# Optimization experiments

Hardware: AMD Instinct MI355X
Metric: run time of the kernel (lower is better)

## Reference

```python
import jax, jax.numpy as jnp
import numpy as np

B, S, D, H = 2, 2048, 512, 8
DK = D // H  # 64


def setup_inputs() -> dict:
    key = jax.random.key(0)
    ks = jax.random.split(key, 16)
    def t(k):
        return jax.random.normal(k, (B, S, D), dtype=jnp.float32)
    inp = {
        'query_real': t(ks[0]), 'key_real': t(ks[1]), 'value_real': t(ks[2]),
        'query_phase': t(ks[3]), 'key_phase': t(ks[4]), 'value_phase': t(ks[5]),
        'mask': jax.random.randint(ks[6], (B, 1, S), 0, 2, dtype=jnp.int32),
    }
    # Four distinct linear layers (clones deepcopies); real and phase paths share them.
    for i, nm in enumerate(['q', 'k', 'v', 'o']):
        inp['W' + nm] = jax.random.normal(ks[7 + 2 * i], (D, D), dtype=jnp.float32) * 0.02
        inp['b' + nm] = jax.random.normal(ks[8 + 2 * i], (D,), dtype=jnp.float32) * 0.02
    return inp


def _lin(x, W, b):
    # nn.Linear: x @ W.T + b
    return jnp.einsum('bsd,ed->bse', x, W) + b


def _heads(x):
    # [B,S,D] -> [B,H,S,DK]
    return jnp.swapaxes(x.reshape(B, S, H, DK), 1, 2)


def reference(query_real, key_real, value_real, query_phase, key_phase, value_phase,
              mask, Wq, bq, Wk, bk, Wv, bv, Wo, bo):
    qr = _heads(_lin(query_real, Wq, bq)); qp = _heads(_lin(query_phase, Wq, bq))
    kr = _heads(_lin(key_real, Wk, bk));   kp = _heads(_lin(key_phase, Wk, bk))
    vr = _heads(_lin(value_real, Wv, bv)); vp = _heads(_lin(value_phase, Wv, bv))

    # complex QK^T: 4 matmuls -> real/imag parts, magnitude score
    sr = jnp.einsum('bhqd,bhkd->bhqk', qr, kr) - jnp.einsum('bhqd,bhkd->bhqk', qp, kp)
    sp = jnp.einsum('bhqd,bhkd->bhqk', qr, kp) + jnp.einsum('bhqd,bhkd->bhqk', qp, kr)
    scores = jnp.sqrt(sr * sr + sp * sp) / jnp.sqrt(jnp.float32(DK))
    # mask [B,1,S] -> unsqueeze head dim -> [B,1,1,S]
    scores = jnp.where(mask[:, None] == 0, jnp.float32(-1e9), scores)
    p = jax.nn.softmax(scores, axis=-1)

    xr = jnp.einsum('bhqk,bhkd->bhqd', p, vr)
    xp = jnp.einsum('bhqk,bhkd->bhqd', p, vp)
    xr = jnp.swapaxes(xr, 1, 2).reshape(B, S, D)
    xp = jnp.swapaxes(xp, 1, 2).reshape(B, S, D)
    return _lin(xr, Wo, bo), _lin(xp, Wo, bo)
```

## Files before the change

### kernel.cpp

```cpp
#include <hip/hip_runtime.h>

typedef __bf16 bf16;
typedef __bf16 bf16x8 __attribute__((ext_vector_type(8)));
typedef float  f32x4  __attribute__((ext_vector_type(4)));

static constexpr int CB = 2;
static constexpr int CS = 2048;
static constexpr int CD = 512;
static constexpr int CH = 8;
static constexpr int CDK = 64;
static constexpr int NROWS = CB * CH * CS;
static constexpr size_t NT = (size_t)CB * CS * CD;
static constexpr size_t WN = (size_t)CD * CD;

__device__ __forceinline__ f32x4 mfma16(bf16x8 a, bf16x8 b, f32x4 c) {
    return __builtin_amdgcn_mfma_f32_16x16x32_bf16(a, b, c, 0, 0, 0);
}

__device__ __forceinline__ bf16x8 cvt8(const float* __restrict__ p) {
    float4 x0 = *reinterpret_cast<const float4*>(p);
    float4 x1 = *reinterpret_cast<const float4*>(p + 4);
    bf16x8 r;
    r[0] = (bf16)x0.x; r[1] = (bf16)x0.y; r[2] = (bf16)x0.z; r[3] = (bf16)x0.w;
    r[4] = (bf16)x1.x; r[5] = (bf16)x1.y; r[6] = (bf16)x1.z; r[7] = (bf16)x1.w;
    return r;
}

__device__ __forceinline__ void gload16(const void* g, void* l) {
    __builtin_amdgcn_global_load_lds(
        (const __attribute__((address_space(1))) void*)g,
        (__attribute__((address_space(3))) void*)l, 16, 0, 0);
}

struct CvtP {
    const float* src[10];
    bf16* dst[10];
    int n8[10];
};
__global__ __launch_bounds__(256) void cvt_kernel(CvtP C) {
    const int t = blockIdx.y;
    const int i = blockIdx.x * 256 + threadIdx.x;
    if (i < C.n8[t])
        *reinterpret_cast<bf16x8*>(C.dst[t] + (size_t)i * 8) =
            cvt8(C.src[t] + (size_t)i * 8);
}

struct PB {
    const bf16* A[6];
    const bf16* W[6];
    const float* bias[6];
    bf16* dst[6];
    int mode[6];
};
__global__ __launch_bounds__(256) void projb_kernel(PB P) {
    __shared__ uint4 tile[2][2][512];

    const int z = blockIdx.z;
    const bf16* __restrict__ A = P.A[z];
    const bf16* __restrict__ W = P.W[z];
    const float* __restrict__ bias = P.bias[z];
    bf16* __restrict__ dst = P.dst[z];
    const int mode = P.mode[z];

    const int m0 = blockIdx.x * 128, n0 = blockIdx.y * 128;
    const int tid = threadIdx.x;
    const int lane = tid & 63, w = tid >> 6;
    const int wr = w >> 1, wc = w & 1;
    const int l16 = lane & 15, lhi = lane >> 4;

    const int tensor = w >> 1, half = w & 1;
    const int rlo = lane >> 2, ch = lane & 3;
    const bf16* gbase = tensor ? W : A;
    const int t0 = tensor ? n0 : m0;
    const char* gp = (const char*)gbase
                   + (size_t)(t0 + half*64 + rlo) * (CD * 2)
                   + (size_t)((ch ^ (rlo & 3)) * 16);

    auto stage = [&](int buf, int kk) {
        const char* p = gp + (size_t)kk * 64;
        uint4* ld = &tile[buf][tensor][half * 256];
        #pragma unroll
        for (int i = 0; i < 4; ++i)
            gload16(p + (size_t)i * 16 * (CD * 2), ld + i * 64);
    };

    f32x4 acc[4][4] = {};

    stage(0, 0);
    asm volatile("s_waitcnt vmcnt(0)" ::: "memory");
    __syncthreads();

    for (int kk = 0; kk < 16; ++kk) {
        if (kk + 1 < 16) stage((kk + 1) & 1, kk + 1);

        const uint4* aT = &tile[kk & 1][0][0];
        const uint4* bT = &tile[kk & 1][1][0];
        bf16x8 af[4], bg[4];
        #pragma unroll
        for (int ms = 0; ms < 4; ++ms) {
            const int ra = wr*64 + ms*16 + l16;
            af[ms] = __builtin_bit_cast(bf16x8, aT[ra*4 + (lhi ^ (ra & 3))]);
        }
        #pragma unroll
        for (int ns = 0; ns < 4; ++ns) {
            const int rb = wc*64 + ns*16 + l16;
            bg[ns] = __builtin_bit_cast(bf16x8, bT[rb*4 + (lhi ^ (rb & 3))]);
        }
        #pragma unroll
        for (int ms = 0; ms < 4; ++ms)
            #pragma unroll
            for (int ns = 0; ns < 4; ++ns)
                acc[ms][ns] = mfma16(af[ms], bg[ns], acc[ms][ns]);

        if (kk + 1 < 16) __syncthreads();
    }

    #pragma unroll
    for (int ms = 0; ms < 4; ++ms)
    #pragma unroll
    for (int ns = 0; ns < 4; ++ns) {
        const int col = n0 + wc*64 + ns*16 + l16;
        const float bv = bias[col];
        const int hh = col >> 6, dk = col & 63;
        #pragma unroll
        for (int i = 0; i < 4; ++i) {
            const int m = m0 + wr*64 + ms*16 + lhi*4 + i;
            const float v = acc[ms][ns][i] + bv;
            const int b = m >> 11, s = m & 2047;
            if (mode == 0)
                dst[(((size_t)(b*CH + hh)) * CS + s) * CDK + dk] = (bf16)v;
            else
                dst[(((size_t)(b*CH + hh)) * CDK + dk) * CS + s] = (bf16)v;
        }
    }
}

__global__ __launch_bounds__(256) void oprojb_kernel(
    const bf16* __restrict__ Xr, const bf16* __restrict__ Xp,
    const bf16* __restrict__ Wo, const float* __restrict__ bo,
    float* __restrict__ out)
{
    __shared__ uint4 tile[2][2][512];

    const bf16* __restrict__ A = blockIdx.z ? Xp : Xr;
    float* __restrict__ dst = out + (size_t)blockIdx.z * NT;

    const int m0 = blockIdx.x * 64, n0 = blockIdx.y * 64;
    const int tid = threadIdx.x;
    const int lane = tid & 63, w = tid >> 6;
    const int wm = w >> 1, wn = w & 1;
    const int l16 = lane & 15, lhi = lane >> 4;

    const int tensor = w >> 1, half = w & 1;
    const int rlo = lane >> 3, slotL = lane & 7;
    const bf16* gbase = tensor ? Wo : A;
    const int t0 = tensor ? n0 : m0;
    const char* gp = (const char*)gbase
                   + (size_t)(t0 + half*32 + rlo) * (CD * 2)
                   + (size_t)((slotL ^ rlo) * 16);

    auto stage = [&](int buf, int kk) {
        const char* p = gp + (size_t)kk * 128;
        uint4* ld = &tile[buf][tensor][half * 256];
        #pragma unroll
        for (int i = 0; i < 4; ++i)
            gload16(p + (size_t)i * 8 * (CD * 2), ld + i * 64);
    };

    f32x4 acc[2][2] = {};

    stage(0, 0);
    asm volatile("s_waitcnt vmcnt(0)" ::: "memory");
    __syncthreads();

    for (int kk = 0; kk < 8; ++kk) {
        if (kk + 1 < 8) stage((kk + 1) & 1, kk + 1);

        const uint4* aT = &tile[kk & 1][0][0];
        const uint4* bT = &tile[kk & 1][1][0];
        #pragma unroll
        for (int ks = 0; ks < 2; ++ks) {
            const int c = ks*4 + lhi;
            const int ra0 = wm*32 + l16, ra1 = ra0 + 16;
            const int rb0 = wn*32 + l16, rb1 = rb0 + 16;
            bf16x8 af0 = __builtin_bit_cast(bf16x8, aT[ra0*8 + (c ^ (ra0 & 7))]);
            bf16x8 af1 = __builtin_bit_cast(bf16x8, aT[ra1*8 + (c ^ (ra1 & 7))]);
            bf16x8 bg0 = __builtin_bit_cast(bf16x8, bT[rb0*8 + (c ^ (rb0 & 7))]);
            bf16x8 bg1 = __builtin_bit_cast(bf16x8, bT[rb1*8 + (c ^ (rb1 & 7))]);
            acc[0][0] = mfma16(af0, bg0, acc[0][0]);
            acc[0][1] = mfma16(af0, bg1, acc[0][1]);
            acc[1][0] = mfma16(af1, bg0, acc[1][0]);
            acc[1][1] = mfma16(af1, bg1, acc[1][1]);
        }
        if (kk + 1 < 8) __syncthreads();
    }

    #pragma unroll
    for (int ms = 0; ms < 2; ++ms)
    #pragma unroll
    for (int ns = 0; ns < 2; ++ns) {
        const int col = n0 + wn*32 + ns*16 + l16;
        const float bv = bo[col];
        #pragma unroll
        for (int i = 0; i < 4; ++i) {
            const int m = m0 + wm*32 + ms*16 + lhi*4 + i;
            dst[(size_t)m * 512 + col] = acc[ms][ns][i] + bv;
        }
    }
}

__global__ __launch_bounds__(512, 4) void attn_kernel(
    const bf16* __restrict__ Qr, const bf16* __restrict__ Qp,
    const bf16* __restrict__ Kr, const bf16* __restrict__ Kp,
    const bf16* __restrict__ Vtr, const bf16* __restrict__ Vtp,
    const int* __restrict__ mask, int lognsp,
    float* __restrict__ POR, float* __restrict__ POP, float* __restrict__ PLs)
{
    __shared__ uint4 stg[2][4][512];

    const int F = blockIdx.x;
    const int qt = (F >> 3) & 15;
    const int g  = (F & 7) | ((F >> 7) << 3);
    const int bh = g >> lognsp, z = g & ((1 << lognsp) - 1);
    const int Lkv = CS >> lognsp, kvbase = z * Lkv;
    const int nt = Lkv >> 6;
    const int b = bh >> 3;
    const size_t base = (size_t)bh * CS * CDK;

    const int tid = threadIdx.x, lane = tid & 63, w = tid >> 6;
    const int l16 = lane & 15, lhi = lane >> 4;
    const int q0 = qt * 128 + w * 16;

    const int tensor = w >> 1, half = w & 1;
    const int rlo = lane >> 3, slotL = lane & 7;
    const int chunkL = slotL ^ rlo;
    const char* gsrc = (tensor == 0) ? (const char*)Kr : (tensor == 1) ? (const char*)Kp
                     : (tensor == 2) ? (const char*)Vtr : (const char*)Vtp;
    size_t laneoff, iStride, tStride;
    if (tensor < 2) {
        laneoff = base*2 + (size_t)(kvbase + half*32 + rlo) * 128 + chunkL*16;
        iStride = 8 * 128;  tStride = 8192;
    } else {
        laneoff = base*2 + (size_t)(half*32 + rlo) * (CS*2) + (size_t)kvbase*2 + chunkL*16;
        iStride = 8 * CS * 2;  tStride = 128;
    }
    const char* gp = gsrc + laneoff;

    auto stage = [&](int bi, int t) {
        const char* p = gp + (size_t)t * tStride;
        uint4* ldst = &stg[bi][tensor][half * 256];
        #pragma unroll
        for (int i = 0; i < 4; ++i)
            gload16(p + i*iStride, ldst + i*64);
    };

    stage(0, 0);

    bf16x8 qrf[2], qpf[2], qnf[2];
    #pragma unroll
    for (int ks = 0; ks < 2; ++ks) {
        const size_t qoff = base + (size_t)(q0 + l16) * CDK + ks*32 + lhi*8;
        qrf[ks] = *reinterpret_cast<const bf16x8*>(&Qr[qoff]);
        qpf[ks] = *reinterpret_cast<const bf16x8*>(&Qp[qoff]);
        uint4 t = __builtin_bit_cast(uint4, qpf[ks]);
        t.x ^= 0x80008000u; t.y ^= 0x80008000u; t.z ^= 0x80008000u; t.w ^= 0x80008000u;
        qnf[ks] = __builtin_bit_cast(bf16x8, t);
    }

    unsigned long long keepA[8] = {};
    for (int t = 0; t < nt; ++t) {
        const unsigned long long m64 =
            __ballot(mask[b*CS + kvbase + t*64 + lane] != 0);
        const unsigned long long s = m64 >> (lhi * 4);
        const unsigned int k16 = (unsigned int)(s & 0xFull)
                               | ((unsigned int)((s >> 16) & 0xFull) << 4)
                               | ((unsigned int)((s >> 32) & 0xFull) << 8)
                               | ((unsigned int)((s >> 48) & 0xFull) << 12);
        keepA[t >> 2] |= (unsigned long long)k16 << ((t & 3) * 16);
    }

    f32x4 oR[4] = {}, oP[4] = {};
    float lpart = 0.f;

    asm volatile("s_waitcnt vmcnt(0)" ::: "memory");
    __syncthreads();

    for (int t = 0; t < nt; ++t) {
        if (t + 1 < nt) stage((t + 1) & 1, t + 1);

        const int bi = t & 1;
        const unsigned int k16 = (unsigned int)(keepA[t >> 2] >> ((t & 3) * 16)) & 0xFFFFu;
        const uint4* kTr = &stg[bi][0][0];
        const uint4* kTp = &stg[bi][1][0];
        const uint4* vTr = &stg[bi][2][0];
        const uint4* vTp = &stg[bi][3][0];

        float pp[4][4];
        #pragma unroll
        for (int kb = 0; kb < 4; ++kb) {
            const int krow = kb*16 + l16;
            f32x4 aR = {}, aP = {};
            __builtin_amdgcn_s_setprio(1);
            #pragma unroll
            for (int ks = 0; ks < 2; ++ks) {
                const int ci = krow*8 + ((ks*4 + lhi) ^ (krow & 7));
                const bf16x8 kr8 = __builtin_bit_cast(bf16x8, kTr[ci]);
                const bf16x8 kp8 = __builtin_bit_cast(bf16x8, kTp[ci]);
                aR = mfma16(kr8, qrf[ks], aR);
                aR = mfma16(kp8, qnf[ks], aR);
                aP = mfma16(kr8, qpf[ks], aP);
                aP = mfma16(kp8, qrf[ks], aP);
            }
            __builtin_amdgcn_s_setprio(0);
            #pragma unroll
            for (int i = 0; i < 4; ++i) {
                const float sr = aR[i], sp = aP[i];
                const float mag = __builtin_amdgcn_sqrtf(fmaf(sr, sr, sp*sp));
                float p = __builtin_amdgcn_exp2f(fmaf(mag, 0.18033688f, -5.77078016f));
                p = ((k16 >> (kb*4 + i)) & 1u) ? p : 0.0f;
                pp[kb][i] = p;
                lpart += p;
            }
        }

        #pragma unroll
        for (int c = 0; c < 2; ++c) {
            unsigned int r0, r1, r2, r3;
            asm("v_cvt_pk_bf16_f32 %0, %1, %2" : "=v"(r0) : "v"(pp[2*c][0]),   "v"(pp[2*c][1]));
            asm("v_cvt_pk_bf16_f32 %0, %1, %2" : "=v"(r1) : "v"(pp[2*c][2]),   "v"(pp[2*c][3]));
            asm("v_cvt_pk_bf16_f32 %0, %1, %2" : "=v"(r2) : "v"(pp[2*c+1][0]), "v"(pp[2*c+1][1]));
            asm("v_cvt_pk_bf16_f32 %0, %1, %2" : "=v"(r3) : "v"(pp[2*c+1][2]), "v"(pp[2*c+1][3]));
            asm volatile("v_permlane32_swap_b32 %0, %1" : "+v"(r0), "+v"(r2));
            asm volatile("v_permlane32_swap_b32 %0, %1" : "+v"(r1), "+v"(r3));
            asm volatile("v_permlane16_swap_b32 %0, %1" : "+v"(r0), "+v"(r2));
            asm volatile("v_permlane16_swap_b32 %0, %1" : "+v"(r1), "+v"(r3));
            uint4 fw; fw.x = r0; fw.y = r1; fw.z = r2; fw.w = r3;
            const bf16x8 pa = __builtin_bit_cast(bf16x8, fw);
            __builtin_amdgcn_s_setprio(1);
            #pragma unroll
            for (int dt = 0; dt < 4; ++dt) {
                const int vrow = dt*16 + l16;
                const int ci = vrow*8 + ((c*4 + lhi) ^ (vrow & 7));
                oR[dt] = mfma16(__builtin_bit_cast(bf16x8, vTr[ci]), pa, oR[dt]);
                oP[dt] = mfma16(__builtin_bit_cast(bf16x8, vTp[ci]), pa, oP[dt]);
            }
            __builtin_amdgcn_s_setprio(0);
        }

        if (t + 1 < nt) __syncthreads();
    }

    {
        float v = lpart;
        v += __shfl_xor(v, 16);
        v += __shfl_xor(v, 32);
        lpart = v;
    }
    const int r0q = bh * CS + q0;
    if (lane < 16)
        PLs[(size_t)z * NROWS + r0q + lane] = lpart;

    const size_t zo = (size_t)z * NROWS * 64;
    #pragma unroll
    for (int dt = 0; dt < 4; ++dt) {
        const size_t off = zo + (size_t)(r0q + l16) * 64 + dt*16 + lhi*4;
        *reinterpret_cast<f32x4*>(&POR[off]) = oR[dt];
        *reinterpret_cast<f32x4*>(&POP[off]) = oP[dt];
    }
}

__global__ __launch_bounds__(256) void merge_kernel(
    const float* __restrict__ POR, const float* __restrict__ POP,
    const float* __restrict__ PLs, int nsp,
    bf16* __restrict__ Xr, bf16* __restrict__ Xp)
{
    const int idx = blockIdx.x * 256 + threadIdx.x;
    const int r = idx >> 4, c0 = (idx & 15) * 4;
    float l = 0.f;
    f32x4 orv = {}, opv = {};
    for (int zz = 0; zz < nsp; ++zz) {
        l += PLs[(size_t)zz * NROWS + r];
        const size_t o = (size_t)zz * NROWS * 64 + (size_t)r * 64 + c0;
        orv += *reinterpret_cast<const f32x4*>(&POR[o]);
        opv += *reinterpret_cast<const f32x4*>(&POP[o]);
    }
    const float inv = 1.f / l;
    const int bh = r >> 11, q = r & 2047;
    const int b = bh >> 3, h = bh & 7;
    const size_t off = ((size_t)(b*CS + q)) * CD + h*CDK + c0;
    bf16 vr[4], vp[4];
    #pragma unroll
    for (int j = 0; j < 4; ++j) { vr[j] = (bf16)(orv[j]*inv); vp[j] = (bf16)(opv[j]*inv); }
    *reinterpret_cast<uint2*>(&Xr[off]) = *reinterpret_cast<const uint2*>(vr);
    *reinterpret_cast<uint2*>(&Xp[off]) = *reinterpret_cast<const uint2*>(vp);
}

extern "C" void kernel_launch(void* const* d_in, const int* in_sizes, int n_in,
                              void* d_out, int out_size, void* d_ws, size_t ws_size,
                              hipStream_t stream) {
    const float* q_r = (const float*)d_in[0];
    const float* k_r = (const float*)d_in[1];
    const float* v_r = (const float*)d_in[2];
    const float* q_p = (const float*)d_in[3];
    const float* k_p = (const float*)d_in[4];
    const float* v_p = (const float*)d_in[5];
    const int*  mask = (const int*)d_in[6];
    const float* Wq = (const float*)d_in[7];  const float* bq = (const float*)d_in[8];
    const float* Wk = (const float*)d_in[9];  const float* bk = (const float*)d_in[10];
    const float* Wv = (const float*)d_in[11]; const float* bv = (const float*)d_in[12];
    const float* Wo = (const float*)d_in[13]; const float* bo = (const float*)d_in[14];
    float* out = (float*)d_out;

    bf16* ws = (bf16*)d_ws;
    bf16* Abf = ws;
    bf16* Wbf = ws + 6 * NT;
    bf16* Qr  = Wbf + 4 * WN;
    bf16 *Qp = Qr + NT, *Kr = Qp + NT, *Kp = Kr + NT;
    bf16 *Vtr = Kp + NT, *Vtp = Vtr + NT;
    bf16 *Xr = Vtp + NT, *Xp = Xr + NT;
    float* POR = (float*)(Xp + NT);

    const size_t fixedB = (14 * NT + 4 * WN) * sizeof(bf16);
    const size_t per_split = (size_t)NROWS * 64 * 4 * 2 + (size_t)NROWS * 4;
    int nsp, lognsp;
    if (ws_size >= fixedB + 2 * per_split) { nsp = 2; lognsp = 1; }
    else                                   { nsp = 1; lognsp = 0; }
    float* POP = POR + (size_t)nsp * NROWS * 64;
    float* PLs = POP + (size_t)nsp * NROWS * 64;

    dim3 blk(256);

    CvtP C;
    C.src[0]=q_r; C.src[1]=q_p; C.src[2]=k_r; C.src[3]=k_p; C.src[4]=v_r; C.src[5]=v_p;
    C.src[6]=Wq;  C.src[7]=Wk;  C.src[8]=Wv;  C.src[9]=Wo;
    for (int i = 0; i < 6; ++i) { C.dst[i] = Abf + (size_t)i * NT; C.n8[i] = (int)(NT / 8); }
    for (int i = 0; i < 4; ++i) { C.dst[6+i] = Wbf + (size_t)i * WN; C.n8[6+i] = (int)(WN / 8); }
    cvt_kernel<<<dim3((unsigned)(NT / 8 / 256), 10), blk, 0, stream>>>(C);

    PB P;
    for (int i = 0; i < 6; ++i) P.A[i] = Abf + (size_t)i * NT;
    P.W[0]=Wbf;      P.W[1]=Wbf;      P.W[2]=Wbf+WN;   P.W[3]=Wbf+WN;
    P.W[4]=Wbf+2*WN; P.W[5]=Wbf+2*WN;
    P.bias[0]=bq; P.bias[1]=bq; P.bias[2]=bk; P.bias[3]=bk; P.bias[4]=bv; P.bias[5]=bv;
    P.dst[0]=Qr; P.dst[1]=Qp; P.dst[2]=Kr; P.dst[3]=Kp; P.dst[4]=Vtr; P.dst[5]=Vtp;
    P.mode[0]=0; P.mode[1]=0; P.mode[2]=0; P.mode[3]=0; P.mode[4]=1; P.mode[5]=1;
    projb_kernel<<<dim3(32, 4, 6), blk, 0, stream>>>(P);

    attn_kernel<<<dim3(256 * nsp), dim3(512), 0, stream>>>(Qr, Qp, Kr, Kp, Vtr, Vtp,
                                                           mask, lognsp, POR, POP, PLs);

    merge_kernel<<<dim3(NROWS * 16 / 256), blk, 0, stream>>>(POR, POP, PLs, nsp, Xr, Xp);

    oprojb_kernel<<<dim3(64, 8, 2), blk, 0, stream>>>(Xr, Xp, Wbf + 3 * WN, bo, out);
}
```

Baseline: 122.0 us.

## Double per-wave query rows, store split partials in bf16, allow four KV splits

Each wave now handles 32 query rows (two 16-row sub-tiles), so every K/V fragment read from LDS feeds twice as many MFMAs. The negation trick moves from Q to K, and the per-block query tile grows to 256 rows, halving the block count per split. The partial outputs written for the split-KV merge drop from fp32 to bf16, and a four-way KV split is enabled when the workspace is large enough. These changes raise register pressure and add bf16 rounding in the partial accumulators.

```diff
diff --git a/kernel.cpp b/kernel.cpp
--- a/kernel.cpp
+++ b/kernel.cpp
@@ -1,6 +1,7 @@
 #include <hip/hip_runtime.h>
 
 typedef __bf16 bf16;
+typedef __bf16 bf16x4 __attribute__((ext_vector_type(4)));
 typedef __bf16 bf16x8 __attribute__((ext_vector_type(8)));
 typedef float  f32x4  __attribute__((ext_vector_type(4)));
 
@@ -214,13 +215,13 @@
     const bf16* __restrict__ Kr, const bf16* __restrict__ Kp,
     const bf16* __restrict__ Vtr, const bf16* __restrict__ Vtp,
     const int* __restrict__ mask, int lognsp,
-    float* __restrict__ POR, float* __restrict__ POP, float* __restrict__ PLs)
+    bf16* __restrict__ POR, bf16* __restrict__ POP, float* __restrict__ PLs)
 {
     __shared__ uint4 stg[2][4][512];
 
     const int F = blockIdx.x;
-    const int qt = (F >> 3) & 15;
-    const int g  = (F & 7) | ((F >> 7) << 3);
+    const int qt = (F >> 3) & 7;
+    const int g  = (F & 7) | ((F >> 6) << 3);
     const int bh = g >> lognsp, z = g & ((1 << lognsp) - 1);
     const int Lkv = CS >> lognsp, kvbase = z * Lkv;
     const int nt = Lkv >> 6;
@@ -229,7 +230,7 @@
 
     const int tid = threadIdx.x, lane = tid & 63, w = tid >> 6;
     const int l16 = lane & 15, lhi = lane >> 4;
-    const int q0 = qt * 128 + w * 16;
+    const int q0 = qt * 256 + w * 32;
 
     const int tensor = w >> 1, half = w & 1;
     const int rlo = lane >> 3, slotL = lane & 7;
@@ -256,16 +257,15 @@
 
     stage(0, 0);
 
-    bf16x8 qrf[2], qpf[2], qnf[2];
-    #pragma unroll
-    for (int ks = 0; ks < 2; ++ks) {
-        const size_t qoff = base + (size_t)(q0 + l16) * CDK + ks*32 + lhi*8;
-        qrf[ks] = *reinterpret_cast<const bf16x8*>(&Qr[qoff]);
-        qpf[ks] = *reinterpret_cast<const bf16x8*>(&Qp[qoff]);
-        uint4 t = __builtin_bit_cast(uint4, qpf[ks]);
-        t.x ^= 0x80008000u; t.y ^= 0x80008000u; t.z ^= 0x80008000u; t.w ^= 0x80008000u;
-        qnf[ks] = __builtin_bit_cast(bf16x8, t);
-    }
+    bf16x8 qrf[2][2], qpf[2][2];
+    #pragma unroll
+    for (int ms = 0; ms < 2; ++ms)
+        #pragma unroll
+        for (int ks = 0; ks < 2; ++ks) {
+            const size_t qoff = base + (size_t)(q0 + ms*16 + l16) * CDK + ks*32 + lhi*8;
+            qrf[ms][ks] = *reinterpret_cast<const bf16x8*>(&Qr[qoff]);
+            qpf[ms][ks] = *reinterpret_cast<const bf16x8*>(&Qp[qoff]);
+        }
 
     unsigned long long keepA[8] = {};
     for (int t = 0; t < nt; ++t) {
@@ -279,8 +279,8 @@
         keepA[t >> 2] |= (unsigned long long)k16 << ((t & 3) * 16);
     }
 
-    f32x4 oR[4] = {}, oP[4] = {};
-    float lpart = 0.f;
+    f32x4 oR[2][4] = {}, oP[2][4] = {};
+    float lpart[2] = {0.f, 0.f};
 
     asm volatile("s_waitcnt vmcnt(0)" ::: "memory");
     __syncthreads();
@@ -295,54 +295,77 @@
         const uint4* vTr = &stg[bi][2][0];
         const uint4* vTp = &stg[bi][3][0];
 
-        float pp[4][4];
+        float pp[2][4][4];
         #pragma unroll
         for (int kb = 0; kb < 4; ++kb) {
             const int krow = kb*16 + l16;
-            f32x4 aR = {}, aP = {};
-            __builtin_amdgcn_s_setprio(1);
+            bf16x8 kr8[2], kp8[2], kn8[2];
             #pragma unroll
             for (int ks = 0; ks < 2; ++ks) {
                 const int ci = krow*8 + ((ks*4 + lhi) ^ (krow & 7));
-                const bf16x8 kr8 = __builtin_bit_cast(bf16x8, kTr[ci]);
-                const bf16x8 kp8 = __builtin_bit_cast(bf16x8, kTp[ci]);
-                aR = mfma16(kr8, qrf[ks], aR);
-                aR = mfma16(kp8, qnf[ks], aR);
-                aP = mfma16(kr8, qpf[ks], aP);
-                aP = mfma16(kp8, qrf[ks], aP);
+                kr8[ks] = __builtin_bit_cast(bf16x8, kTr[ci]);
+                kp8[ks] = __builtin_bit_cast(bf16x8, kTp[ci]);
+                uint4 tn = __builtin_bit_cast(uint4, kp8[ks]);
+                tn.x ^= 0x80008000u; tn.y ^= 0x80008000u;
+                tn.z ^= 0x80008000u; tn.w ^= 0x80008000u;
+                kn8[ks] = __builtin_bit_cast(bf16x8, tn);
             }
-            __builtin_amdgcn_s_setprio(0);
-            #pragma unroll
-            for (int i = 0; i < 4; ++i) {
-                const float sr = aR[i], sp = aP[i];
-                const float mag = __builtin_amdgcn_sqrtf(fmaf(sr, sr, sp*sp));
-                float p = __builtin_amdgcn_exp2f(fmaf(mag, 0.18033688f, -5.77078016f));
-                p = ((k16 >> (kb*4 + i)) & 1u) ? p : 0.0f;
-                pp[kb][i] = p;
-                lpart += p;
+            #pragma unroll
+            for (int ms = 0; ms < 2; ++ms) {
+                f32x4 aR = {}, aP = {};
+                __builtin_amdgcn_s_setprio(1);
+                #pragma unroll
+                for (int ks = 0; ks < 2; ++ks) {
+                    aR = mfma16(kr8[ks], qrf[ms][ks], aR);
+                    aR = mfma16(kn8[ks], qpf[ms][ks], aR);
+                    aP = mfma16(kr8[ks], qpf[ms][ks], aP);
+                    aP = mfma16(kp8[ks], qrf[ms][ks], aP);
+                }
+                __builtin_amdgcn_s_setprio(0);
+                #pragma unroll
+                for (int i = 0; i < 4; ++i) {
+                    const float sr = aR[i], sp = aP[i];
+                    const float mag = __builtin_amdgcn_sqrtf(fmaf(sr, sr, sp*sp));
+                    float p = __builtin_amdgcn_exp2f(fmaf(mag, 0.18033688f, -5.77078016f));
+                    p = ((k16 >> (kb*4 + i)) & 1u) ? p : 0.0f;
+                    pp[ms][kb][i] = p;
+                    lpart[ms] += p;
+                }
             }
         }
 
+        bf16x8 pa[2][2];
+        #pragma unroll
+        for (int c = 0; c < 2; ++c)
+            #pragma unroll
+            for (int ms = 0; ms < 2; ++ms) {
+                unsigned int r0, r1, r2, r3;
+                asm("v_cvt_pk_bf16_f32 %0, %1, %2" : "=v"(r0) : "v"(pp[ms][2*c][0]),   "v"(pp[ms][2*c][1]));
+                asm("v_cvt_pk_bf16_f32 %0, %1, %2" : "=v"(r1) : "v"(pp[ms][2*c][2]),   "v"(pp[ms][2*c][3]));
+                asm("v_cvt_pk_bf16_f32 %0, %1, %2" : "=v"(r2) : "v"(pp[ms][2*c+1][0]), "v"(pp[ms][2*c+1][1]));
+                asm("v_cvt_pk_bf16_f32 %0, %1, %2" : "=v"(r3) : "v"(pp[ms][2*c+1][2]), "v"(pp[ms][2*c+1][3]));
+                asm volatile("v_permlane32_swap_b32 %0, %1" : "+v"(r0), "+v"(r2));
+                asm volatile("v_permlane32_swap_b32 %0, %1" : "+v"(r1), "+v"(r3));
+                asm volatile("v_permlane16_swap_b32 %0, %1" : "+v"(r0), "+v"(r2));
+                asm volatile("v_permlane16_swap_b32 %0, %1" : "+v"(r1), "+v"(r3));
+                uint4 fw; fw.x = r0; fw.y = r1; fw.z = r2; fw.w = r3;
+                pa[c][ms] = __builtin_bit_cast(bf16x8, fw);
+            }
+
         #pragma unroll
         for (int c = 0; c < 2; ++c) {
-            unsigned int r0, r1, r2, r3;
-            asm("v_cvt_pk_bf16_f32 %0, %1, %2" : "=v"(r0) : "v"(pp[2*c][0]),   "v"(pp[2*c][1]));
-            asm("v_cvt_pk_bf16_f32 %0, %1, %2" : "=v"(r1) : "v"(pp[2*c][2]),   "v"(pp[2*c][3]));
-            asm("v_cvt_pk_bf16_f32 %0, %1, %2" : "=v"(r2) : "v"(pp[2*c+1][0]), "v"(pp[2*c+1][1]));
-            asm("v_cvt_pk_bf16_f32 %0, %1, %2" : "=v"(r3) : "v"(pp[2*c+1][2]), "v"(pp[2*c+1][3]));
-            asm volatile("v_permlane32_swap_b32 %0, %1" : "+v"(r0), "+v"(r2));
-            asm volatile("v_permlane32_swap_b32 %0, %1" : "+v"(r1), "+v"(r3));
-            asm volatile("v_permlane16_swap_b32 %0, %1" : "+v"(r0), "+v"(r2));
-            asm volatile("v_permlane16_swap_b32 %0, %1" : "+v"(r1), "+v"(r3));
-            uint4 fw; fw.x = r0; fw.y = r1; fw.z = r2; fw.w = r3;
-            const bf16x8 pa = __builtin_bit_cast(bf16x8, fw);
             __builtin_amdgcn_s_setprio(1);
             #pragma unroll
             for (int dt = 0; dt < 4; ++dt) {
                 const int vrow = dt*16 + l16;
                 const int ci = vrow*8 + ((c*4 + lhi) ^ (vrow & 7));
-                oR[dt] = mfma16(__builtin_bit_cast(bf16x8, vTr[ci]), pa, oR[dt]);
-                oP[dt] = mfma16(__builtin_bit_cast(bf16x8, vTp[ci]), pa, oP[dt]);
+                const bf16x8 v8r = __builtin_bit_cast(bf16x8, vTr[ci]);
+                const bf16x8 v8p = __builtin_bit_cast(bf16x8, vTp[ci]);
+                #pragma unroll
+                for (int ms = 0; ms < 2; ++ms) {
+                    oR[ms][dt] = mfma16(v8r, pa[c][ms], oR[ms][dt]);
+                    oP[ms][dt] = mfma16(v8p, pa[c][ms], oP[ms][dt]);
+                }
             }
             __builtin_amdgcn_s_setprio(0);
         }
@@ -350,27 +373,37 @@
         if (t + 1 < nt) __syncthreads();
     }
 
-    {
-        float v = lpart;
+    #pragma unroll
+    for (int ms = 0; ms < 2; ++ms) {
+        float v = lpart[ms];
         v += __shfl_xor(v, 16);
         v += __shfl_xor(v, 32);
-        lpart = v;
+        lpart[ms] = v;
     }
     const int r0q = bh * CS + q0;
-    if (lane < 16)
-        PLs[(size_t)z * NROWS + r0q + lane] = lpart;
-
+    if (lane < 16) {
+        PLs[(size_t)z * NROWS + r0q + lane]      = lpart[0];
+        PLs[(size_t)z * NROWS + r0q + 16 + lane] = lpart[1];
+    }
     const size_t zo = (size_t)z * NROWS * 64;
     #pragma unroll
-    for (int dt = 0; dt < 4; ++dt) {
-        const size_t off = zo + (size_t)(r0q + l16) * 64 + dt*16 + lhi*4;
-        *reinterpret_cast<f32x4*>(&POR[off]) = oR[dt];
-        *reinterpret_cast<f32x4*>(&POP[off]) = oP[dt];
-    }
+    for (int ms = 0; ms < 2; ++ms)
+        #pragma unroll
+        for (int dt = 0; dt < 4; ++dt) {
+            const size_t off = zo + (size_t)(r0q + ms*16 + l16) * 64 + dt*16 + lhi*4;
+            bf16 t4r[4], t4p[4];
+            #pragma unroll
+            for (int i = 0; i < 4; ++i) {
+                t4r[i] = (bf16)oR[ms][dt][i];
+                t4p[i] = (bf16)oP[ms][dt][i];
+            }
+            *reinterpret_cast<uint2*>(&POR[off]) = *reinterpret_cast<const uint2*>(t4r);
+            *reinterpret_cast<uint2*>(&POP[off]) = *reinterpret_cast<const uint2*>(t4p);
+        }
 }
 
 __global__ __launch_bounds__(256) void merge_kernel(
-    const float* __restrict__ POR, const float* __restrict__ POP,
+    const bf16* __restrict__ POR, const bf16* __restrict__ POP,
     const float* __restrict__ PLs, int nsp,
     bf16* __restrict__ Xr, bf16* __restrict__ Xp)
 {
@@ -381,8 +414,10 @@
     for (int zz = 0; zz < nsp; ++zz) {
         l += PLs[(size_t)zz * NROWS + r];
         const size_t o = (size_t)zz * NROWS * 64 + (size_t)r * 64 + c0;
-        orv += *reinterpret_cast<const f32x4*>(&POR[o]);
-        opv += *reinterpret_cast<const f32x4*>(&POP[o]);
+        const bf16x4 a = *reinterpret_cast<const bf16x4*>(&POR[o]);
+        const bf16x4 bq = *reinterpret_cast<const bf16x4*>(&POP[o]);
+        #pragma unroll
+        for (int j = 0; j < 4; ++j) { orv[j] += (float)a[j]; opv[j] += (float)bq[j]; }
     }
     const float inv = 1.f / l;
     const int bh = r >> 11, q = r & 2047;
@@ -418,15 +453,16 @@
     bf16 *Qp = Qr + NT, *Kr = Qp + NT, *Kp = Kr + NT;
     bf16 *Vtr = Kp + NT, *Vtp = Vtr + NT;
     bf16 *Xr = Vtp + NT, *Xp = Xr + NT;
-    float* POR = (float*)(Xp + NT);
+    bf16* POR = Xp + NT;
 
     const size_t fixedB = (14 * NT + 4 * WN) * sizeof(bf16);
-    const size_t per_split = (size_t)NROWS * 64 * 4 * 2 + (size_t)NROWS * 4;
+    const size_t per_split = (size_t)NROWS * 64 * 2 * 2 + (size_t)NROWS * 4;
     int nsp, lognsp;
-    if (ws_size >= fixedB + 2 * per_split) { nsp = 2; lognsp = 1; }
-    else                                   { nsp = 1; lognsp = 0; }
-    float* POP = POR + (size_t)nsp * NROWS * 64;
-    float* PLs = POP + (size_t)nsp * NROWS * 64;
+    if (ws_size >= fixedB + 4 * per_split)      { nsp = 4; lognsp = 2; }
+    else if (ws_size >= fixedB + 2 * per_split) { nsp = 2; lognsp = 1; }
+    else                                        { nsp = 1; lognsp = 0; }
+    bf16* POP = POR + (size_t)nsp * NROWS * 64;
+    float* PLs = (float*)(POP + (size_t)nsp * NROWS * 64);
 
     dim3 blk(256);
 
@@ -446,7 +482,7 @@
     P.mode[0]=0; P.mode[1]=0; P.mode[2]=0; P.mode[3]=0; P.mode[4]=1; P.mode[5]=1;
     projb_kernel<<<dim3(32, 4, 6), blk, 0, stream>>>(P);
 
-    attn_kernel<<<dim3(256 * nsp), dim3(512), 0, stream>>>(Qr, Qp, Kr, Kp, Vtr, Vtp,
+    attn_kernel<<<dim3(128 * nsp), dim3(512), 0, stream>>>(Qr, Qp, Kr, Kp, Vtr, Vtp,
                                                            mask, lognsp, POR, POP, PLs);
 
     merge_kernel<<<dim3(NROWS * 16 / 256), blk, 0, stream>>>(POR, POP, PLs, nsp, Xr, Xp);
```

Result: slower. 317.1 us (+159.9%).
